# Performance work log

Hardware: AMD Instinct MI355X
Metric: run time of the kernel (lower is better)

Reference implementation:

```python
import jax, jax.numpy as jnp
import numpy as np

B, N, E = 2, 30000, 120000
IN_F, OUT_F, H = 512, 512, 4
D = OUT_F // H  # head_dim = 128
LN_EPS = 1e-5


def setup_inputs() -> dict:
    key = jax.random.key(0)
    k1, k2, k3, k4 = jax.random.split(key, 4)
    node_features = jax.random.normal(k1, (B, N, IN_F), dtype=jnp.float32)
    edge_index = jax.random.randint(k2, (2, E), 0, N, dtype=jnp.int64)
    # per-head linear transforms (bias=False): W[h] is [in_features, head_dim]
    W = jax.random.normal(k3, (H, IN_F, D), dtype=jnp.float32) / np.sqrt(IN_F)
    # per-head attention vectors a[h] is [2*head_dim] (Linear(2*head_dim,1,bias=False))
    a = jax.random.normal(k4, (H, 2 * D), dtype=jnp.float32) / np.sqrt(2 * D)
    ln_gamma = jnp.ones((OUT_F,), dtype=jnp.float32)
    ln_beta = jnp.zeros((OUT_F,), dtype=jnp.float32)
    return {"node_features": node_features, "edge_index": edge_index,
            "W": W, "a": a, "ln_gamma": ln_gamma, "ln_beta": ln_beta}


def reference(node_features, edge_index, W, a, ln_gamma, ln_beta):
    src, dst = edge_index[0], edge_index[1]
    # all-heads linear transform: [B, H, N, D]
    t = jnp.einsum('bni,hid->bhnd', node_features, W)
    # per-edge gathered features: [B, H, E, D]
    sf = t[:, :, src, :]
    df = t[:, :, dst, :]
    # attention score = [sf ; df] . a  == sf.a_src + df.a_dst  -> [B, H, E]
    scores = (jnp.einsum('bhed,hd->bhe', sf, a[:, :D])
              + jnp.einsum('bhed,hd->bhe', df, a[:, D:]))
    scores = jax.nn.leaky_relu(scores, negative_slope=0.2)
    # NOTE: faithful to source — softmax over ALL edges (dim=-1), not per-dst
    w = jax.nn.softmax(scores, axis=-1)
    # scatter-add aggregation into destination nodes (the Python-loop in torch)
    agg = jnp.zeros_like(t).at[:, :, dst, :].add(w[..., None] * sf)  # [B,H,N,D]
    # concat heads along feature dim (head order preserved)
    out = jnp.transpose(agg, (0, 2, 1, 3)).reshape(node_features.shape[0], N, H * D)
    # LayerNorm over last dim
    mu = jnp.mean(out, axis=-1, keepdims=True)
    var = jnp.mean(jnp.square(out - mu), axis=-1, keepdims=True)
    out = (out - mu) * jax.lax.rsqrt(var + LN_EPS) * ln_gamma + ln_beta
    return out
```

## Files before the change

kernel.cpp:

```cpp
#include <hip/hip_runtime.h>
#include <stdint.h>

#define Bn 2
#define Nn 30000
#define En 120000
#define KIN 512
#define Hh 4
#define Dd 128
#define MROWS 60000
#define MPAD  60032
#define LNEPS 1e-5f
#define EBLK 469

typedef unsigned short u16;
typedef unsigned int   u32;
typedef __attribute__((ext_vector_type(8))) short short8;
typedef __attribute__((ext_vector_type(4))) float f32x4;

__device__ __forceinline__ u16 f2bf(float f) {
    u32 u = __builtin_bit_cast(u32, f);
    u32 r = u + 0x7FFFu + ((u >> 16) & 1u);
    return (u16)(r >> 16);
}
__device__ __forceinline__ float bflo(u32 u) {
    return __builtin_bit_cast(float, u << 16);
}
__device__ __forceinline__ float bfhi(u32 u) {
    return __builtin_bit_cast(float, u & 0xFFFF0000u);
}
__device__ __forceinline__ void ld16(void* lds, const void* g) {
    __builtin_amdgcn_global_load_lds((const __attribute__((address_space(1))) void*)g,
                                     (__attribute__((address_space(3))) void*)lds, 16, 0, 0);
}

#define CVTX_BLKS 15008
#define CVTW_BLKS 1024
__global__ void prep_kernel(const float* __restrict__ x, u16* __restrict__ xb,
                            const float* __restrict__ W, u16* __restrict__ wbt,
                            const int* __restrict__ ei, int* __restrict__ deg) {
    int blk = blockIdx.x;
    if (blk < CVTX_BLKS) {
        long base = ((long)blk * 256 + threadIdx.x) * 8;
        short8 o = {};
        if (base < (long)MROWS * KIN) {
            const float4* px = (const float4*)(x + base);
            float4 v0 = px[0], v1 = px[1];
            o[0] = (short)f2bf(v0.x); o[1] = (short)f2bf(v0.y);
            o[2] = (short)f2bf(v0.z); o[3] = (short)f2bf(v0.w);
            o[4] = (short)f2bf(v1.x); o[5] = (short)f2bf(v1.y);
            o[6] = (short)f2bf(v1.z); o[7] = (short)f2bf(v1.w);
        }
        *(short8*)(xb + base) = o;
    } else if (blk < CVTX_BLKS + CVTW_BLKS) {
        int idx = (blk - CVTX_BLKS) * 256 + threadIdx.x;
        int c = idx >> 9, i = idx & 511;
        int h = c >> 7, d = c & 127;
        wbt[idx] = f2bf(W[h * (KIN * Dd) + i * Dd + d]);
    } else {
        int e = (blk - CVTX_BLKS - CVTW_BLKS) * 256 + threadIdx.x;
        if (e < En) atomicAdd(&deg[ei[En + e]], 1);
    }
}

__device__ void scan512(const int* __restrict__ deg, int* __restrict__ offs,
                        int* __restrict__ cursor) {
    __shared__ int part[512];
    int tid = threadIdx.x;
    const int CH = 59;
    int start = tid * CH;
    int s = 0;
    for (int i = 0; i < CH; i++) {
        int n = start + i;
        if (n < Nn) s += deg[n];
    }
    part[tid] = s;
    __syncthreads();
    for (int off = 1; off < 512; off <<= 1) {
        int xv = (tid >= off) ? part[tid - off] : 0;
        __syncthreads();
        part[tid] += xv;
        __syncthreads();
    }
    int run = part[tid] - s;
    for (int i = 0; i < CH; i++) {
        int n = start + i;
        if (n < Nn) {
            offs[n] = run;
            cursor[n] = run;
            run += deg[n];
        }
    }
    if (tid == 511) offs[Nn] = part[511];
}

__launch_bounds__(512)
__global__ void gemm(const u16* __restrict__ xb, const u16* __restrict__ wbt,
                     const float* __restrict__ ag, u16* __restrict__ t,
                     float* __restrict__ s1g, float* __restrict__ s2g,
                     const int* __restrict__ deg, int* __restrict__ offs,
                     int* __restrict__ cursor) {
    if (blockIdx.x == 0) { scan512(deg, offs, cursor); return; }
    __shared__ __align__(16) u16 As[2][128 * 32];
    __shared__ __align__(16) u16 Bs[2][512 * 32];
    const int tid = threadIdx.x;
    const int m0 = (blockIdx.x - 1) * 128;
    const int w = tid >> 6, l = tid & 63;
    const int lr = l & 15, lk = l >> 4;
    const int wrM = (w >> 2) * 64;
    const int h = w & 3;
    const int wc = h * 128;
    const int swz = (lk * 8) ^ ((lr & 6) << 2);
    int aoff[4], boff[8];
    #pragma unroll
    for (int mi = 0; mi < 4; mi++) aoff[mi] = (wrM + mi * 16 + lr) * 32 + swz;
    #pragma unroll
    for (int nj = 0; nj < 8; nj++) boff[nj] = (wc + nj * 16 + lr) * 32 + swz;

    const int grow = tid >> 2, gslot = tid & 3;
    const int gsw = (gslot * 8) ^ ((grow & 6) << 2);
    const u16* agsrc = xb + (long)(m0 + grow) * KIN + gsw;
    const u16* bgsrc = wbt + (long)grow * KIN + gsw;
    f32x4 acc[4][8] = {};

    auto STAGE = [&](u16* Ab, u16* Bb, int k0) {
        ld16(Ab + (long)tid * 8, agsrc + k0);
        #pragma unroll
        for (int i = 0; i < 4; i++)
            ld16(Bb + ((long)(i * 512 + tid)) * 8, bgsrc + (long)i * 128 * KIN + k0);
    };

    STAGE(As[0], Bs[0], 0);
    __syncthreads();
    #pragma unroll 2
    for (int t16 = 0; t16 < 16; t16++) {
        u16* Ac = As[t16 & 1];
        u16* Bc = Bs[t16 & 1];
        if (t16 < 15) STAGE(As[(t16 + 1) & 1], Bs[(t16 + 1) & 1], (t16 + 1) * 32);
        short8 af[4];
        #pragma unroll
        for (int mi = 0; mi < 4; mi++) af[mi] = *(const short8*)&Ac[aoff[mi]];
        #pragma unroll
        for (int nj = 0; nj < 8; nj++) {
            short8 bv = *(const short8*)&Bc[boff[nj]];
            #pragma unroll
            for (int mi = 0; mi < 4; mi++)
                acc[mi][nj] = __builtin_amdgcn_mfma_f32_16x16x32_bf16(
                    af[mi], bv, acc[mi][nj], 0, 0, 0);
        }
        __syncthreads();
    }
    #pragma unroll
    for (int mi = 0; mi < 4; mi++)
        #pragma unroll
        for (int r = 0; r < 4; r++) {
            int row = m0 + wrM + mi * 16 + lk * 4 + r;
            u16* tp = t + (long)row * 512 + wc + lr;
            #pragma unroll
            for (int nj = 0; nj < 8; nj++)
                tp[nj * 16] = f2bf(acc[mi][nj][r]);
        }
    float a1c[8], a2c[8];
    #pragma unroll
    for (int nj = 0; nj < 8; nj++) {
        int col = nj * 16 + lr;
        a1c[nj] = ag[h * 256 + col];
        a2c[nj] = ag[h * 256 + 128 + col];
    }
    float p1[16], p2[16];
    #pragma unroll
    for (int mi = 0; mi < 4; mi++)
        #pragma unroll
        for (int r = 0; r < 4; r++) {
            float v1 = 0.f, v2 = 0.f;
            #pragma unroll
            for (int nj = 0; nj < 8; nj++) {
                float tv = acc[mi][nj][r];
                v1 += tv * a1c[nj];
                v2 += tv * a2c[nj];
            }
            p1[mi * 4 + r] = v1;
            p2[mi * 4 + r] = v2;
        }
    #pragma unroll
    for (int off = 1; off < 16; off <<= 1)
        #pragma unroll
        for (int i = 0; i < 16; i++) {
            p1[i] += __shfl_xor(p1[i], off, 64);
            p2[i] += __shfl_xor(p2[i], off, 64);
        }
    if (lr == 0) {
        #pragma unroll
        for (int mi = 0; mi < 4; mi++)
            #pragma unroll
            for (int r = 0; r < 4; r++) {
                int row = m0 + wrM + mi * 16 + lk * 4 + r;
                if (row < MROWS) {
                    s1g[(long)row * 4 + h] = p1[mi * 4 + r];
                    s2g[(long)row * 4 + h] = p2[mi * 4 + r];
                }
            }
    }
}

__global__ void edgescatter_kernel(const int* __restrict__ ei, const float* __restrict__ s1,
                                   const float* __restrict__ s2, int* __restrict__ cursor,
                                   int* __restrict__ srcs, float* __restrict__ pw,
                                   float* __restrict__ Zpart) {
    int e = blockIdx.x * 256 + threadIdx.x;
    int tid = threadIdx.x;
    float v[8] = {0.f, 0.f, 0.f, 0.f, 0.f, 0.f, 0.f, 0.f};
    if (e < En) {
        int src = ei[e], dst = ei[En + e];
        #pragma unroll
        for (int b = 0; b < Bn; b++) {
            float4 v1 = *(const float4*)(s1 + ((long)b * Nn + src) * 4);
            float4 v2 = *(const float4*)(s2 + ((long)b * Nn + dst) * 4);
            float s;
            s = v1.x + v2.x; s = s > 0.f ? s : 0.2f * s; v[b * 4 + 0] = __expf(s);
            s = v1.y + v2.y; s = s > 0.f ? s : 0.2f * s; v[b * 4 + 1] = __expf(s);
            s = v1.z + v2.z; s = s > 0.f ? s : 0.2f * s; v[b * 4 + 2] = __expf(s);
            s = v1.w + v2.w; s = s > 0.f ? s : 0.2f * s; v[b * 4 + 3] = __expf(s);
        }
        int pos = atomicAdd(&cursor[dst], 1);
        srcs[pos] = src;
        *(float4*)(pw + (long)pos * 4)        = make_float4(v[0], v[1], v[2], v[3]);
        *(float4*)(pw + ((long)En + pos) * 4) = make_float4(v[4], v[5], v[6], v[7]);
    }
    #pragma unroll
    for (int off = 1; off < 64; off <<= 1)
        #pragma unroll
        for (int i = 0; i < 8; i++)
            v[i] += __shfl_xor(v[i], off, 64);
    __shared__ float red[4][8];
    if ((tid & 63) == 0)
        #pragma unroll
        for (int i = 0; i < 8; i++)
            red[tid >> 6][i] = v[i];
    __syncthreads();
    if (tid < 8)
        Zpart[(long)blockIdx.x * 8 + tid] =
            red[0][tid] + red[1][tid] + red[2][tid] + red[3][tid];
}

__global__ void zreduce_kernel(const float* __restrict__ Zpart, float* __restrict__ invZ) {
    int tid = threadIdx.x;
    int g = tid >> 5, l = tid & 31;
    float s = 0.f;
    for (int i = l; i < EBLK; i += 32)
        s += Zpart[(long)i * 8 + g];
    #pragma unroll
    for (int off = 1; off < 32; off <<= 1)
        s += __shfl_xor(s, off, 64);
    if (l == 0) invZ[g] = 1.0f / s;
}

__launch_bounds__(128)
__global__ void agg_kernel(const u16* __restrict__ t, const int* __restrict__ srcs,
                           const float* __restrict__ pw, const float* __restrict__ invZ,
                           const int* __restrict__ offs,
                           const float* __restrict__ gamma, const float* __restrict__ beta,
                           float* __restrict__ out) {
    int tid = threadIdx.x;
    int n = blockIdx.x;
    int b = blockIdx.y;
    int h = tid >> 5;
    int j0 = offs[n], j1 = offs[n + 1];
    const float* pwb = pw + (long)b * En * 4;
    const u16* tb = t + (long)b * Nn * 512;
    float a0 = 0.f, a1 = 0.f, a2 = 0.f, a3 = 0.f;
    int j = j0;
    for (; j + 4 <= j1; j += 4) {
        int s0 = srcs[j], s1i = srcs[j + 1], s2i = srcs[j + 2], s3i = srcs[j + 3];
        float w0 = pwb[(long)j * 4 + h];
        float w1 = pwb[(long)(j + 1) * 4 + h];
        float w2 = pwb[(long)(j + 2) * 4 + h];
        float w3 = pwb[(long)(j + 3) * 4 + h];
        uint2 r0 = *(const uint2*)(tb + (long)s0 * 512 + tid * 4);
        uint2 r1 = *(const uint2*)(tb + (long)s1i * 512 + tid * 4);
        uint2 r2 = *(const uint2*)(tb + (long)s2i * 512 + tid * 4);
        uint2 r3 = *(const uint2*)(tb + (long)s3i * 512 + tid * 4);
        a0 += w0 * bflo(r0.x) + w1 * bflo(r1.x) + w2 * bflo(r2.x) + w3 * bflo(r3.x);
        a1 += w0 * bfhi(r0.x) + w1 * bfhi(r1.x) + w2 * bfhi(r2.x) + w3 * bfhi(r3.x);
        a2 += w0 * bflo(r0.y) + w1 * bflo(r1.y) + w2 * bflo(r2.y) + w3 * bflo(r3.y);
        a3 += w0 * bfhi(r0.y) + w1 * bfhi(r1.y) + w2 * bfhi(r2.y) + w3 * bfhi(r3.y);
    }
    for (; j < j1; j++) {
        int s0 = srcs[j];
        float w0 = pwb[(long)j * 4 + h];
        uint2 r0 = *(const uint2*)(tb + (long)s0 * 512 + tid * 4);
        a0 += w0 * bflo(r0.x);
        a1 += w0 * bfhi(r0.x);
        a2 += w0 * bflo(r0.y);
        a3 += w0 * bfhi(r0.y);
    }
    float invz = invZ[b * 4 + h];
    a0 *= invz; a1 *= invz; a2 *= invz; a3 *= invz;
    float s  = a0 + a1 + a2 + a3;
    float ss = a0 * a0 + a1 * a1 + a2 * a2 + a3 * a3;
    #pragma unroll
    for (int off = 1; off < 64; off <<= 1) {
        s  += __shfl_xor(s, off, 64);
        ss += __shfl_xor(ss, off, 64);
    }
    __shared__ float red[2][2];
    int wv = tid >> 6;
    if ((tid & 63) == 0) { red[wv][0] = s; red[wv][1] = ss; }
    __syncthreads();
    s  = red[0][0] + red[1][0];
    ss = red[0][1] + red[1][1];
    float mean = s * (1.0f / 512.0f);
    float var = ss * (1.0f / 512.0f) - mean * mean;
    var = var < 0.f ? 0.f : var;
    float scale = rsqrtf(var + LNEPS);
    int c = tid * 4;
    float4 o;
    o.x = (a0 - mean) * scale * gamma[c + 0] + beta[c + 0];
    o.y = (a1 - mean) * scale * gamma[c + 1] + beta[c + 1];
    o.z = (a2 - mean) * scale * gamma[c + 2] + beta[c + 2];
    o.w = (a3 - mean) * scale * gamma[c + 3] + beta[c + 3];
    *(float4*)(out + ((long)b * Nn + n) * 512 + c) = o;
}

extern "C" void kernel_launch(void* const* d_in, const int* in_sizes, int n_in,
                              void* d_out, int out_size, void* d_ws, size_t ws_size,
                              hipStream_t stream) {
    const float* x     = (const float*)d_in[0];
    const int*   ei    = (const int*)d_in[1];
    const float* W     = (const float*)d_in[2];
    const float* a     = (const float*)d_in[3];
    const float* gamma = (const float*)d_in[4];
    const float* beta  = (const float*)d_in[5];
    float* out = (float*)d_out;

    char* ws = (char*)d_ws;
    size_t off = 0;
    auto alloc = [&](size_t bytes) -> void* {
        void* ptr = ws + off;
        off = (off + bytes + 255) & ~(size_t)255;
        return ptr;
    };
    u16*   xb     = (u16*)alloc((size_t)MPAD * KIN * 2);
    u16*   wbt    = (u16*)alloc((size_t)512 * 512 * 2);
    u16*   t      = (u16*)alloc((size_t)MPAD * 512 * 2);
    float* s1     = (float*)alloc((size_t)MROWS * 4 * 4);
    float* s2     = (float*)alloc((size_t)MROWS * 4 * 4);
    float* pw     = (float*)alloc((size_t)Bn * En * 4 * 4);
    float* Zpart  = (float*)alloc((size_t)EBLK * 8 * 4);
    float* invZ   = (float*)alloc(8 * 4);
    int*   deg    = (int*)alloc((size_t)Nn * 4);
    int*   offs   = (int*)alloc((size_t)(Nn + 1) * 4);
    int*   cursor = (int*)alloc((size_t)Nn * 4);
    int*   srcs   = (int*)alloc((size_t)En * 4);

    hipMemsetAsync(deg, 0, (size_t)Nn * 4, stream);

    prep_kernel<<<CVTX_BLKS + CVTW_BLKS + EBLK, 256, 0, stream>>>(x, xb, W, wbt, ei, deg);
    gemm<<<470, 512, 0, stream>>>(xb, wbt, a, t, s1, s2, deg, offs, cursor);
    edgescatter_kernel<<<EBLK, 256, 0, stream>>>(ei, s1, s2, cursor, srcs, pw, Zpart);
    zreduce_kernel<<<1, 256, 0, stream>>>(Zpart, invZ);
    agg_kernel<<<dim3(Nn, Bn), 128, 0, stream>>>(t, srcs, pw, invZ, offs, gamma, beta, out);
}
```

Baseline: 396.7 us.

## Load GEMM fragments directly from global memory into registers, dropping LDS staging

The GEMM no longer stages A and B tiles in LDS through global_load_lds with barriers. Each wave now loads its MFMA fragments straight from global memory into registers, double-buffered across K steps, and launch bounds request two blocks per CU. This removes LDS traffic and __syncthreads, but waves sharing a tile now load the same data redundantly. Those duplicate reads rely on L2/L1 hits, and register pressure rises under the tighter occupancy bound.

```diff
diff --git a/kernel.cpp b/kernel.cpp
--- a/kernel.cpp
+++ b/kernel.cpp
@@ -27,10 +27,6 @@
 }
 __device__ __forceinline__ float bfhi(u32 u) {
     return __builtin_bit_cast(float, u & 0xFFFF0000u);
-}
-__device__ __forceinline__ void ld16(void* lds, const void* g) {
-    __builtin_amdgcn_global_load_lds((const __attribute__((address_space(1))) void*)g,
-                                     (__attribute__((address_space(3))) void*)lds, 16, 0, 0);
 }
 
 #define CVTX_BLKS 15008
@@ -93,15 +89,13 @@
     if (tid == 511) offs[Nn] = part[511];
 }
 
-__launch_bounds__(512)
+__launch_bounds__(512, 2)
 __global__ void gemm(const u16* __restrict__ xb, const u16* __restrict__ wbt,
                      const float* __restrict__ ag, u16* __restrict__ t,
                      float* __restrict__ s1g, float* __restrict__ s2g,
                      const int* __restrict__ deg, int* __restrict__ offs,
                      int* __restrict__ cursor) {
     if (blockIdx.x == 0) { scan512(deg, offs, cursor); return; }
-    __shared__ __align__(16) u16 As[2][128 * 32];
-    __shared__ __align__(16) u16 Bs[2][512 * 32];
     const int tid = threadIdx.x;
     const int m0 = (blockIdx.x - 1) * 128;
     const int w = tid >> 6, l = tid & 63;
@@ -109,46 +103,49 @@
     const int wrM = (w >> 2) * 64;
     const int h = w & 3;
     const int wc = h * 128;
-    const int swz = (lk * 8) ^ ((lr & 6) << 2);
-    int aoff[4], boff[8];
-    #pragma unroll
-    for (int mi = 0; mi < 4; mi++) aoff[mi] = (wrM + mi * 16 + lr) * 32 + swz;
-    #pragma unroll
-    for (int nj = 0; nj < 8; nj++) boff[nj] = (wc + nj * 16 + lr) * 32 + swz;
-
-    const int grow = tid >> 2, gslot = tid & 3;
-    const int gsw = (gslot * 8) ^ ((grow & 6) << 2);
-    const u16* agsrc = xb + (long)(m0 + grow) * KIN + gsw;
-    const u16* bgsrc = wbt + (long)grow * KIN + gsw;
+
+    const u16* abase[4];
+    const u16* bbase[8];
+    #pragma unroll
+    for (int mi = 0; mi < 4; mi++)
+        abase[mi] = xb + (long)(m0 + wrM + mi * 16 + lr) * KIN + lk * 8;
+    #pragma unroll
+    for (int nj = 0; nj < 8; nj++)
+        bbase[nj] = wbt + (long)(wc + nj * 16 + lr) * KIN + lk * 8;
+
     f32x4 acc[4][8] = {};
-
-    auto STAGE = [&](u16* Ab, u16* Bb, int k0) {
-        ld16(Ab + (long)tid * 8, agsrc + k0);
-        #pragma unroll
-        for (int i = 0; i < 4; i++)
-            ld16(Bb + ((long)(i * 512 + tid)) * 8, bgsrc + (long)i * 128 * KIN + k0);
-    };
-
-    STAGE(As[0], Bs[0], 0);
-    __syncthreads();
-    #pragma unroll 2
-    for (int t16 = 0; t16 < 16; t16++) {
-        u16* Ac = As[t16 & 1];
-        u16* Bc = Bs[t16 & 1];
-        if (t16 < 15) STAGE(As[(t16 + 1) & 1], Bs[(t16 + 1) & 1], (t16 + 1) * 32);
-        short8 af[4];
-        #pragma unroll
-        for (int mi = 0; mi < 4; mi++) af[mi] = *(const short8*)&Ac[aoff[mi]];
-        #pragma unroll
-        for (int nj = 0; nj < 8; nj++) {
-            short8 bv = *(const short8*)&Bc[boff[nj]];
-            #pragma unroll
-            for (int mi = 0; mi < 4; mi++)
-                acc[mi][nj] = __builtin_amdgcn_mfma_f32_16x16x32_bf16(
-                    af[mi], bv, acc[mi][nj], 0, 0, 0);
-        }
-        __syncthreads();
-    }
+    short8 afA[4], bfA[8], afB[4], bfB[8];
+
+#define LOADF(AF, BF, KS)                                           \
+    {                                                               \
+        _Pragma("unroll")                                           \
+        for (int mi = 0; mi < 4; mi++)                              \
+            AF[mi] = *(const short8*)(abase[mi] + (KS) * 32);       \
+        _Pragma("unroll")                                           \
+        for (int nj = 0; nj < 8; nj++)                              \
+            BF[nj] = *(const short8*)(bbase[nj] + (KS) * 32);       \
+    }
+#define MFMAF(AF, BF)                                               \
+    {                                                               \
+        _Pragma("unroll")                                           \
+        for (int nj = 0; nj < 8; nj++)                              \
+            _Pragma("unroll")                                       \
+            for (int mi = 0; mi < 4; mi++)                          \
+                acc[mi][nj] = __builtin_amdgcn_mfma_f32_16x16x32_bf16( \
+                    AF[mi], BF[nj], acc[mi][nj], 0, 0, 0);          \
+    }
+
+    LOADF(afA, bfA, 0);
+    #pragma unroll
+    for (int t16 = 0; t16 < 16; t16 += 2) {
+        LOADF(afB, bfB, t16 + 1);
+        MFMAF(afA, bfA);
+        if (t16 < 14) LOADF(afA, bfA, t16 + 2);
+        MFMAF(afB, bfB);
+    }
+#undef LOADF
+#undef MFMAF
+
     #pragma unroll
     for (int mi = 0; mi < 4; mi++)
         #pragma unroll
```

Result: no change. 396.4 us (-0.1%).
